# Kernel optimization log

Hardware: AMD Instinct MI355X
Metric: run time of the kernel (lower is better)

## Reference

```python
import jax, jax.numpy as jnp
import numpy as np

EPS_LN = 1e-5


def layer_norm(x, g, b):
    mu = jnp.mean(x, axis=-1, keepdims=True)
    var = jnp.mean((x - mu) ** 2, axis=-1, keepdims=True)
    return (x - mu) * jax.lax.rsqrt(var + EPS_LN) * g + b


def setup_inputs() -> dict:
    key = jax.random.key(0)
    ks = jax.random.split(key, 16)
    N, E, H, EA = 25000, 400000, 128, 1
    h = jax.random.normal(ks[0], (N, H), dtype=jnp.float32)
    coord = jax.random.normal(ks[1], (N, 3), dtype=jnp.float32)
    edge_index = jax.random.randint(ks[2], (2, E), 0, N, dtype=jnp.int64)
    edge_attr = jax.random.normal(ks[3], (E, EA), dtype=jnp.float32)

    def lin(k, fan_in, fan_out):
        lim = 1.0 / np.sqrt(fan_in)
        return jax.random.uniform(k, (fan_in, fan_out), jnp.float32, -lim, lim)

    in_edge = 2 * H + 1 + EA  # 258
    params = {
        'e_W1': lin(ks[4], in_edge, H), 'e_b1': jnp.zeros((H,), jnp.float32),
        'e_g1': jnp.ones((H,), jnp.float32), 'e_be1': jnp.zeros((H,), jnp.float32),
        'e_W2': lin(ks[5], H, H), 'e_b2': jnp.zeros((H,), jnp.float32),
        'e_g2': jnp.ones((H,), jnp.float32), 'e_be2': jnp.zeros((H,), jnp.float32),
        'n_W1': lin(ks[6], 2 * H, H), 'n_b1': jnp.zeros((H,), jnp.float32),
        'n_g1': jnp.ones((H,), jnp.float32), 'n_be1': jnp.zeros((H,), jnp.float32),
        'n_W2': lin(ks[7], H, H), 'n_b2': jnp.zeros((H,), jnp.float32),
        'c_W1': lin(ks[8], H, H), 'c_b1': jnp.zeros((H,), jnp.float32),
        'c_g1': jnp.ones((H,), jnp.float32), 'c_be1': jnp.zeros((H,), jnp.float32),
        # xavier_uniform with gain=0.001, no bias
        'c_W2': jax.random.uniform(ks[9], (H, 1), jnp.float32, -1.0, 1.0) * (0.001 * np.sqrt(6.0 / (H + 1))),
    }
    return dict(h=h, edge_index=edge_index, coord=coord, edge_attr=edge_attr, **params)


def reference(h, edge_index, coord, edge_attr,
              e_W1, e_b1, e_g1, e_be1, e_W2, e_b2, e_g2, e_be2,
              n_W1, n_b1, n_g1, n_be1, n_W2, n_b2,
              c_W1, c_b1, c_g1, c_be1, c_W2):
    N = h.shape[0]
    row, col = edge_index[0], edge_index[1]

    coord_diff = coord[row] - coord[col]                     # [E,3]
    radial = jnp.sum(coord_diff ** 2, axis=1, keepdims=True)  # [E,1]
    norm = jnp.sqrt(radial + 1e-8)
    coord_diff = coord_diff / (norm + 1.0)

    inp = jnp.concatenate([h[row], h[col], radial, edge_attr], axis=1)  # [E,258]
    x = jax.nn.silu(layer_norm(inp @ e_W1 + e_b1, e_g1, e_be1))
    edge_feat = jax.nn.silu(layer_norm(x @ e_W2 + e_b2, e_g2, e_be2))   # [E,H]

    cm = jax.nn.silu(layer_norm(edge_feat @ c_W1 + c_b1, c_g1, c_be1)) @ c_W2  # [E,1]
    trans = coord_diff * cm                                   # [E,3]

    coord_out = coord + jax.ops.segment_sum(trans, row, num_segments=N)
    agg = jax.ops.segment_sum(edge_feat, row, num_segments=N)  # [N,H]

    node_in = jnp.concatenate([h, agg], axis=1)               # [N,2H]
    out = jax.nn.silu(layer_norm(node_in @ n_W1 + n_b1, n_g1, n_be1)) @ n_W2 + n_b2
    out = h + out  # recurrent
    return out, coord_out
```

## Files before the change

kernel.cpp:

```cpp
#include <hip/hip_runtime.h>
#include <math.h>

#define H 128
#define KE 256
#define KN 256
#define XSTR 136
#define SSTR 132

typedef __attribute__((ext_vector_type(8))) short bf16x8;
typedef __attribute__((ext_vector_type(4))) float f32x4;

__device__ __forceinline__ float fast_rcp(float x) {
#if defined(__has_builtin) && __has_builtin(__builtin_amdgcn_rcpf)
    return __builtin_amdgcn_rcpf(x);
#else
    return 1.0f / x;
#endif
}
__device__ __forceinline__ float fast_rsq(float x) {
#if defined(__has_builtin) && __has_builtin(__builtin_amdgcn_rsqf)
    return __builtin_amdgcn_rsqf(x);
#else
    return rsqrtf(x);
#endif
}
__device__ __forceinline__ float fast_sqrt(float x) {
#if defined(__has_builtin) && __has_builtin(__builtin_amdgcn_sqrtf)
    return __builtin_amdgcn_sqrtf(x);
#else
    return sqrtf(x);
#endif
}

__device__ __forceinline__ float silu_f(float x) {
    return x * fast_rcp(1.0f + __expf(-x));
}

__device__ __forceinline__ unsigned short f2bf(float f) {
    unsigned int u = __float_as_uint(f);
    unsigned int r = u + 0x7FFFu + ((u >> 16) & 1u);
    return (unsigned short)(r >> 16);
}

__device__ __forceinline__ unsigned int pkbf(float a, float b) {
#if defined(__has_builtin)
#if __has_builtin(__builtin_amdgcn_cvt_pk_bf16_f32)
    typedef __attribute__((ext_vector_type(2))) __bf16 bf16x2_t;
    bf16x2_t v = __builtin_amdgcn_cvt_pk_bf16_f32(a, b);
    return *(unsigned int*)&v;
#else
    return (unsigned int)f2bf(a) | ((unsigned int)f2bf(b) << 16);
#endif
#else
    return (unsigned int)f2bf(a) | ((unsigned int)f2bf(b) << 16);
#endif
}

__device__ __forceinline__ float bflo(unsigned int w) { return __uint_as_float(w << 16); }
__device__ __forceinline__ float bfhi(unsigned int w) { return __uint_as_float(w & 0xFFFF0000u); }

__device__ __forceinline__ void atomic_pk_add_bf16(unsigned short* addr, unsigned int pkv) {
    asm volatile("global_atomic_pk_add_bf16 %0, %1, off"
                 :: "v"(addr), "v"(pkv) : "memory");
}

template<int CTRL>
__device__ __forceinline__ float dpp_add(float x) {
    int t = __builtin_amdgcn_update_dpp(0, __float_as_int(x), CTRL, 0xF, 0xF, true);
    return x + __int_as_float(t);
}
__device__ __forceinline__ float red16(float x) {
    x = dpp_add<0x128>(x);
    x = dpp_add<0x124>(x);
    x = dpp_add<0x122>(x);
    x = dpp_add<0x121>(x);
    return x;
}

__device__ __forceinline__ void wfrag(const float* __restrict__ W,
                                      unsigned short* __restrict__ Wf, int f) {
    int kb = f >> 9, rem = f & 511;
    int nt = rem >> 6, lane = rem & 63;
    int quad = lane >> 4, l15 = lane & 15;
    int n = nt * 16 + l15, k0 = kb * 32 + quad * 8;
    union { bf16x8 v; unsigned short u[8]; } pk;
    #pragma unroll
    for (int j = 0; j < 8; ++j) pk.u[j] = f2bf(W[(size_t)(k0 + j) * H + n]);
    *(bf16x8*)&Wf[(size_t)f * 8] = pk.v;
}

__global__ __launch_bounds__(256) void prep_all(
    const float* __restrict__ h, unsigned short* __restrict__ hb, int n4_h,
    float* __restrict__ aggz, int n4_agg,
    const float* __restrict__ coord, float* __restrict__ coord_out, int n_coord,
    const float* __restrict__ eW1, const float* __restrict__ eW2,
    const float* __restrict__ cW1, const float* __restrict__ nW1,
    const float* __restrict__ nW2,
    unsigned short* __restrict__ eW1f, unsigned short* __restrict__ eW2f,
    unsigned short* __restrict__ cW1f, unsigned short* __restrict__ nW1f,
    unsigned short* __restrict__ nW2f,
    int b0, int b1, int b2)
{
    int b = blockIdx.x;
    int t = threadIdx.x;
    if (b < b0) {
        int i = b * 256 + t;
        if (i < n4_h) {
            float4 f = ((const float4*)h)[i];
            ((uint2*)hb)[i] = make_uint2(pkbf(f.x, f.y), pkbf(f.z, f.w));
        }
    } else if (b < b1) {
        int i = (b - b0) * 256 + t;
        if (i < n4_agg) ((float4*)aggz)[i] = (float4){0.f, 0.f, 0.f, 0.f};
    } else if (b < b2) {
        int i = (b - b1) * 256 + t;
        if (i < n_coord) coord_out[i] = coord[i];
    } else {
        int idx = (b - b2) * 256 + t;
        if      (idx <  4096) wfrag(eW1, eW1f, idx);
        else if (idx <  8192) wfrag(nW1, nW1f, idx - 4096);
        else if (idx < 10240) wfrag(eW2, eW2f, idx - 8192);
        else if (idx < 12288) wfrag(cW1, cW1f, idx - 10240);
        else if (idx < 14336) wfrag(nW2, nW2f, idx - 12288);
    }
}

__global__ __launch_bounds__(256, 4) void proj_kernel(
    const unsigned short* __restrict__ hb,
    const unsigned short* __restrict__ eW1f,
    unsigned short* __restrict__ Pb, int N)
{
    __shared__ unsigned short Ys[4][16 * 256];

    const int wv = threadIdx.x >> 6;
    const int lane = threadIdx.x & 63;
    const int l15 = lane & 15, quad = lane >> 4;
    const int gn0 = (blockIdx.x * 4 + wv) * 16;
    unsigned short* Y = &Ys[wv][0];

    if (gn0 >= N) return;
    int nl = gn0 + l15; if (nl >= N) nl = N - 1;

    f32x4 a1[8], a2[8];
    #pragma unroll
    for (int nt = 0; nt < 8; ++nt) {
        a1[nt] = (f32x4){0.f, 0.f, 0.f, 0.f};
        a2[nt] = (f32x4){0.f, 0.f, 0.f, 0.f};
    }

    for (int kb = 0; kb < 4; ++kb) {
        int ko = kb * 32 + quad * 8;
        bf16x8 af = *(const bf16x8*)(hb + (size_t)nl * H + ko);
        const unsigned short* bp1 = eW1f + ((size_t)kb * 8) * 512 + (size_t)lane * 8;
        const unsigned short* bp2 = eW1f + ((size_t)(kb + 4) * 8) * 512 + (size_t)lane * 8;
        #pragma unroll
        for (int nt = 0; nt < 8; ++nt) {
            bf16x8 b1 = *(const bf16x8*)(bp1 + (size_t)nt * 512);
            bf16x8 b2 = *(const bf16x8*)(bp2 + (size_t)nt * 512);
            a1[nt] = __builtin_amdgcn_mfma_f32_16x16x32_bf16(af, b1, a1[nt], 0, 0, 0);
            a2[nt] = __builtin_amdgcn_mfma_f32_16x16x32_bf16(af, b2, a2[nt], 0, 0, 0);
        }
    }

    #pragma unroll
    for (int nt = 0; nt < 8; ++nt) {
        int c = nt * 16 + l15;
        #pragma unroll
        for (int r = 0; r < 4; ++r) {
            int rr = quad * 4 + r;
            Y[rr * 256 + c]       = f2bf(a1[nt][r]);
            Y[rr * 256 + 128 + c] = f2bf(a2[nt][r]);
        }
    }

    const int m = lane >> 2, part = lane & 3;
    int gm = gn0 + m; if (gm >= N) gm = N - 1;
    #pragma unroll
    for (int j = 0; j < 8; ++j) {
        uint4 v = *(const uint4*)&Y[m * 256 + part * 64 + j * 8];
        *(uint4*)(Pb + (size_t)gm * 256 + part * 64 + j * 8) = v;
    }
}

__device__ __forceinline__ void ln_silu_store1(
    f32x4* acc, const float* __restrict__ bias, const float* __restrict__ g,
    const float* __restrict__ be, unsigned short* X, int l15, int quad)
{
    float s[4] = {0,0,0,0}, q[4] = {0,0,0,0};
    #pragma unroll
    for (int nt = 0; nt < 8; ++nt) {
        float b = bias[nt * 16 + l15];
        #pragma unroll
        for (int r = 0; r < 4; ++r) {
            float x = acc[nt][r] + b; acc[nt][r] = x; s[r] += x; q[r] += x * x;
        }
    }
    #pragma unroll
    for (int r = 0; r < 4; ++r) { s[r] = red16(s[r]); q[r] = red16(q[r]); }
    #pragma unroll
    for (int r = 0; r < 4; ++r) {
        float mu = s[r] * 0.0078125f, v = q[r] * 0.0078125f - mu * mu;
        s[r] = mu; q[r] = fast_rsq(v + 1e-5f);
    }
    #pragma unroll
    for (int nt = 0; nt < 8; ++nt) {
        float gg = g[nt * 16 + l15], bb = be[nt * 16 + l15];
        #pragma unroll
        for (int r = 0; r < 4; ++r) {
            float a = q[r] * gg, c = bb - s[r] * a;
            float y = silu_f(fmaf(acc[nt][r], a, c));
            acc[nt][r] = y;
            X[(quad * 4 + r) * XSTR + nt * 16 + l15] = f2bf(y);
        }
    }
}

__global__ __launch_bounds__(64, 4) void edge_kernel(
    const unsigned short* __restrict__ Pb, const int* __restrict__ ei,
    const float* __restrict__ coord, const float* __restrict__ eattr,
    const float* __restrict__ eW1,
    const float* __restrict__ eb1, const float* __restrict__ eg1, const float* __restrict__ ebe1,
    const unsigned short* __restrict__ eW2f,
    const float* __restrict__ eb2, const float* __restrict__ eg2, const float* __restrict__ ebe2,
    const unsigned short* __restrict__ cW1f,
    const float* __restrict__ cb1, const float* __restrict__ cg1, const float* __restrict__ cbe1,
    const float* __restrict__ cW2,
    unsigned short* __restrict__ aggb, float* __restrict__ coord_out, int E)
{
    __shared__ float S[16 * SSTR];
    unsigned short* X = (unsigned short*)S;

    const int lane = threadIdx.x;
    const int l15 = lane & 15, quad = lane >> 4;
    const int ge0 = blockIdx.x * 16;

    int el  = ge0 + l15;
    int elc = (el < E) ? el : (E - 1);
    int rowl = ei[elc], coll = ei[E + elc];
    float dx = coord[rowl * 3 + 0] - coord[coll * 3 + 0];
    float dy = coord[rowl * 3 + 1] - coord[coll * 3 + 1];
    float dz = coord[rowl * 3 + 2] - coord[coll * 3 + 2];
    float radial = dx * dx + dy * dy + dz * dz;
    float inv = fast_rcp(fast_sqrt(radial + 1e-8f) + 1.0f);
    float cdx = dx * inv, cdy = dy * inv, cdz = dz * inv;
    float ea = eattr[elc];

    {
        const int m = lane >> 2, part = lane & 3;
        int row_m = __shfl(rowl, m, 64);
        int col_m = __shfl(coll, m, 64);
        const unsigned short* p1 = Pb + (size_t)row_m * 256 + part * 32;
        const unsigned short* p2 = Pb + (size_t)col_m * 256 + 128 + part * 32;
        #pragma unroll
        for (int j = 0; j < 4; ++j) {
            uint4 a = *(const uint4*)(p1 + j * 8);
            uint4 b = *(const uint4*)(p2 + j * 8);
            float4 v0, v1;
            v0.x = bflo(a.x) + bflo(b.x); v0.y = bfhi(a.x) + bfhi(b.x);
            v0.z = bflo(a.y) + bflo(b.y); v0.w = bfhi(a.y) + bfhi(b.y);
            v1.x = bflo(a.z) + bflo(b.z); v1.y = bfhi(a.z) + bfhi(b.z);
            v1.z = bflo(a.w) + bflo(b.w); v1.w = bfhi(a.w) + bfhi(b.w);
            *(float4*)&S[m * SSTR + part * 32 + j * 8]     = v0;
            *(float4*)&S[m * SSTR + part * 32 + j * 8 + 4] = v1;
        }
    }

    f32x4 acc[8];
    {
        float rad_r[4], ea_r[4];
        #pragma unroll
        for (int r = 0; r < 4; ++r) {
            rad_r[r] = __shfl(radial, quad * 4 + r, 64);
            ea_r[r]  = __shfl(ea,     quad * 4 + r, 64);
        }
        #pragma unroll
        for (int nt = 0; nt < 8; ++nt) {
            float w256 = eW1[256 * H + nt * 16 + l15];
            float w257 = eW1[257 * H + nt * 16 + l15];
            #pragma unroll
            for (int r = 0; r < 4; ++r) {
                float base = S[(quad * 4 + r) * SSTR + nt * 16 + l15];
                acc[nt][r] = base + rad_r[r] * w256 + ea_r[r] * w257;
            }
        }
    }

    ln_silu_store1(acc, eb1, eg1, ebe1, X, l15, quad);

    f32x4 ac2[8];
    #pragma unroll
    for (int nt = 0; nt < 8; ++nt) ac2[nt] = (f32x4){0.f, 0.f, 0.f, 0.f};
    for (int kb = 0; kb < 4; ++kb) {
        bf16x8 af = *(const bf16x8*)&X[l15 * XSTR + kb * 32 + quad * 8];
        const unsigned short* bp = eW2f + ((size_t)kb * 8) * 512 + (size_t)lane * 8;
        #pragma unroll
        for (int nt = 0; nt < 8; ++nt) {
            bf16x8 bf = *(const bf16x8*)(bp + (size_t)nt * 512);
            ac2[nt] = __builtin_amdgcn_mfma_f32_16x16x32_bf16(af, bf, ac2[nt], 0, 0, 0);
        }
    }

    ln_silu_store1(ac2, eb2, eg2, ebe2, X, l15, quad);

    {
        int rowm[4];
        #pragma unroll
        for (int r = 0; r < 4; ++r) rowm[r] = __shfl(rowl, quad * 4 + r, 64);
        #pragma unroll
        for (int c4 = 0; c4 < 4; ++c4) {
            #pragma unroll
            for (int r = 0; r < 4; ++r) {
                int geh = ge0 + quad * 4 + r;
                if (geh < E) {
                    unsigned int pkv =
                        *(const unsigned int*)&X[(quad * 4 + r) * XSTR + c4 * 32 + 2 * l15];
                    atomic_pk_add_bf16(aggb + (size_t)rowm[r] * H + c4 * 32 + 2 * l15, pkv);
                }
            }
        }
    }

    f32x4 acc3[8];
    #pragma unroll
    for (int nt = 0; nt < 8; ++nt) acc3[nt] = (f32x4){0.f, 0.f, 0.f, 0.f};
    for (int kb = 0; kb < 4; ++kb) {
        bf16x8 af = *(const bf16x8*)&X[l15 * XSTR + kb * 32 + quad * 8];
        const unsigned short* bp = cW1f + ((size_t)kb * 8) * 512 + (size_t)lane * 8;
        #pragma unroll
        for (int nt = 0; nt < 8; ++nt) {
            bf16x8 bf = *(const bf16x8*)(bp + (size_t)nt * 512);
            acc3[nt] = __builtin_amdgcn_mfma_f32_16x16x32_bf16(af, bf, acc3[nt], 0, 0, 0);
        }
    }

    {
        float s[4] = {0,0,0,0}, q[4] = {0,0,0,0};
        #pragma unroll
        for (int nt = 0; nt < 8; ++nt) {
            float b = cb1[nt * 16 + l15];
            #pragma unroll
            for (int r = 0; r < 4; ++r) {
                float x = acc3[nt][r] + b; acc3[nt][r] = x; s[r] += x; q[r] += x * x;
            }
        }
        #pragma unroll
        for (int r = 0; r < 4; ++r) { s[r] = red16(s[r]); q[r] = red16(q[r]); }
        #pragma unroll
        for (int r = 0; r < 4; ++r) {
            float mu = s[r] * 0.0078125f, v = q[r] * 0.0078125f - mu * mu;
            s[r] = mu; q[r] = fast_rsq(v + 1e-5f);
        }
        float cm[4] = {0,0,0,0};
        #pragma unroll
        for (int nt = 0; nt < 8; ++nt) {
            float gg = cg1[nt * 16 + l15], bb = cbe1[nt * 16 + l15];
            float w2 = cW2[nt * 16 + l15];
            #pragma unroll
            for (int r = 0; r < 4; ++r) {
                float a = q[r] * gg, c = bb - s[r] * a;
                cm[r] += silu_f(fmaf(acc3[nt][r], a, c)) * w2;
            }
        }
        #pragma unroll
        for (int r = 0; r < 4; ++r) cm[r] = red16(cm[r]);
        #pragma unroll
        for (int r = 0; r < 4; ++r) {
            int src = quad * 4 + r;
            float cdxr = __shfl(cdx, src, 64);
            float cdyr = __shfl(cdy, src, 64);
            float cdzr = __shfl(cdz, src, 64);
            int rw = __shfl(rowl, src, 64);
            float comp = (l15 == 0) ? cdxr : ((l15 == 1) ? cdyr : cdzr);
            int geh = ge0 + src;
            if (l15 < 3 && geh < E)
                atomicAdd(&coord_out[(size_t)rw * 3 + l15], comp * cm[r]);
        }
    }
}

__global__ __launch_bounds__(256, 4) void node_kernel(
    const unsigned short* __restrict__ hb, const float* __restrict__ h,
    const unsigned short* __restrict__ aggb,
    const unsigned short* __restrict__ nW1f,
    const float* __restrict__ nb1, const float* __restrict__ ng1, const float* __restrict__ nbe1,
    const unsigned short* __restrict__ nW2f, const float* __restrict__ nb2,
    float* __restrict__ out, int N)
{
    __shared__ unsigned short Xs[4][16 * XSTR];

    const int wv   = threadIdx.x >> 6;
    const int lane = threadIdx.x & 63;
    const int l15 = lane & 15, quad = lane >> 4;
    const int gn0 = (blockIdx.x * 4 + wv) * 16;
    unsigned short* X = &Xs[wv][0];

    if (gn0 >= N) return;
    int nl = gn0 + l15; if (nl >= N) nl = N - 1;

    f32x4 acc[8];
    #pragma unroll
    for (int nt = 0; nt < 8; ++nt) acc[nt] = (f32x4){0.f, 0.f, 0.f, 0.f};

    for (int kb = 0; kb < 8; ++kb) {
        int ko = (kb & 3) * 32 + quad * 8;
        const unsigned short* src = (kb < 4) ? hb : aggb;
        bf16x8 af = *(const bf16x8*)(src + (size_t)nl * H + ko);
        const unsigned short* bp = nW1f + ((size_t)kb * 8) * 512 + (size_t)lane * 8;
        #pragma unroll
        for (int nt = 0; nt < 8; ++nt) {
            bf16x8 bf = *(const bf16x8*)(bp + (size_t)nt * 512);
            acc[nt] = __builtin_amdgcn_mfma_f32_16x16x32_bf16(af, bf, acc[nt], 0, 0, 0);
        }
    }

    ln_silu_store1(acc, nb1, ng1, nbe1, X, l15, quad);

    f32x4 ac2[8];
    #pragma unroll
    for (int nt = 0; nt < 8; ++nt) ac2[nt] = (f32x4){0.f, 0.f, 0.f, 0.f};
    for (int kb = 0; kb < 4; ++kb) {
        bf16x8 af = *(const bf16x8*)&X[l15 * XSTR + kb * 32 + quad * 8];
        const unsigned short* bp = nW2f + ((size_t)kb * 8) * 512 + (size_t)lane * 8;
        #pragma unroll
        for (int nt = 0; nt < 8; ++nt) {
            bf16x8 bf = *(const bf16x8*)(bp + (size_t)nt * 512);
            ac2[nt] = __builtin_amdgcn_mfma_f32_16x16x32_bf16(af, bf, ac2[nt], 0, 0, 0);
        }
    }

    #pragma unroll
    for (int nt = 0; nt < 8; ++nt) {
        float b = nb2[nt * 16 + l15];
        #pragma unroll
        for (int r = 0; r < 4; ++r) {
            int gn = gn0 + quad * 4 + r;
            if (gn < N) {
                size_t idx = (size_t)gn * H + nt * 16 + l15;
                out[idx] = ac2[nt][r] + b + h[idx];
            }
        }
    }
}

extern "C" void kernel_launch(void* const* d_in, const int* in_sizes, int n_in,
                              void* d_out, int out_size, void* d_ws, size_t ws_size,
                              hipStream_t stream) {
    const float* h     = (const float*)d_in[0];
    const int*   ei    = (const int*)d_in[1];
    const float* coord = (const float*)d_in[2];
    const float* eattr = (const float*)d_in[3];
    const float* eW1   = (const float*)d_in[4];
    const float* eb1   = (const float*)d_in[5];
    const float* eg1   = (const float*)d_in[6];
    const float* ebe1  = (const float*)d_in[7];
    const float* eW2   = (const float*)d_in[8];
    const float* eb2   = (const float*)d_in[9];
    const float* eg2   = (const float*)d_in[10];
    const float* ebe2  = (const float*)d_in[11];
    const float* nW1   = (const float*)d_in[12];
    const float* nb1   = (const float*)d_in[13];
    const float* ng1   = (const float*)d_in[14];
    const float* nbe1  = (const float*)d_in[15];
    const float* nW2   = (const float*)d_in[16];
    const float* nb2   = (const float*)d_in[17];
    const float* cW1   = (const float*)d_in[18];
    const float* cb1   = (const float*)d_in[19];
    const float* cg1   = (const float*)d_in[20];
    const float* cbe1  = (const float*)d_in[21];
    const float* cW2   = (const float*)d_in[22];

    const int N = in_sizes[0] / H;
    const int E = in_sizes[1] / 2;

    float* out       = (float*)d_out;
    float* coord_out = out + (size_t)N * H;

    char* ws = (char*)d_ws;
    size_t o = 0;
    unsigned short* aggb = (unsigned short*)(ws + o); o += (size_t)N * H * 2;
    unsigned short* hb   = (unsigned short*)(ws + o); o += (size_t)N * H * 2;
    unsigned short* Pb   = (unsigned short*)(ws + o); o += (size_t)N * 256 * 2;
    unsigned short* eW1f = (unsigned short*)(ws + o); o += (size_t)H * KE * 2;
    unsigned short* eW2f = (unsigned short*)(ws + o); o += (size_t)H * H * 2;
    unsigned short* cW1f = (unsigned short*)(ws + o); o += (size_t)H * H * 2;
    unsigned short* nW1f = (unsigned short*)(ws + o); o += (size_t)H * KN * 2;
    unsigned short* nW2f = (unsigned short*)(ws + o); o += (size_t)H * H * 2;

    const int n4_h   = N * H / 4;
    const int n4_agg = N * H / 8;
    const int n_co   = N * 3;
    const int b0 = (n4_h   + 255) / 256;
    const int b1 = b0 + (n4_agg + 255) / 256;
    const int b2 = b1 + (n_co   + 255) / 256;
    const int bw = (4096 + 4096 + 2048 + 2048 + 2048 + 255) / 256;
    prep_all<<<b2 + bw, 256, 0, stream>>>(
        h, hb, n4_h, (float*)aggb, n4_agg, coord, coord_out, n_co,
        eW1, eW2, cW1, nW1, nW2,
        eW1f, eW2f, cW1f, nW1f, nW2f, b0, b1, b2);

    proj_kernel<<<(N + 63) / 64, 256, 0, stream>>>(hb, eW1f, Pb, N);

    edge_kernel<<<(E + 15) / 16, 64, 0, stream>>>(
        Pb, ei, coord, eattr,
        eW1, eb1, eg1, ebe1,
        eW2f, eb2, eg2, ebe2,
        cW1f, cb1, cg1, cbe1, cW2,
        aggb, coord_out, E);

    node_kernel<<<(N + 63) / 64, 256, 0, stream>>>(
        hb, h, aggb, nW1f, nb1, ng1, nbe1, nW2f, nb2, out, N);
}
```

Before: 301.2 us.

## Pack two waves per edge block and stage layer-1 input as bf16

The edge kernel now runs two independent 16-edge waves per 128-thread block, each with its own bf16 LDS tile, instead of one wave per block. The radial and edge_attr terms of the first layer are folded in during the gather, and the pre-activation is stored as bf16 in the shared X buffer rather than as an fp32 staging array. This shrinks LDS per wave and raises launch bounds to allow more resident waves. In exchange the layer-1 pre-activation is rounded to bf16 before layer norm, which costs some accuracy.

```diff
diff --git a/kernel.cpp b/kernel.cpp
--- a/kernel.cpp
+++ b/kernel.cpp
@@ -5,7 +5,6 @@
 #define KE 256
 #define KN 256
 #define XSTR 136
-#define SSTR 132
 
 typedef __attribute__((ext_vector_type(8))) short bf16x8;
 typedef __attribute__((ext_vector_type(4))) float f32x4;
@@ -58,6 +57,9 @@
 
 __device__ __forceinline__ float bflo(unsigned int w) { return __uint_as_float(w << 16); }
 __device__ __forceinline__ float bfhi(unsigned int w) { return __uint_as_float(w & 0xFFFF0000u); }
+__device__ __forceinline__ float bfu(unsigned short u) {
+    return __uint_as_float((unsigned int)u << 16);
+}
 
 __device__ __forceinline__ void atomic_pk_add_bf16(unsigned short* addr, unsigned int pkv) {
     asm volatile("global_atomic_pk_add_bf16 %0, %1, off"
@@ -215,7 +217,7 @@
     }
 }
 
-__global__ __launch_bounds__(64, 4) void edge_kernel(
+__global__ __launch_bounds__(128, 8) void edge_kernel(
     const unsigned short* __restrict__ Pb, const int* __restrict__ ei,
     const float* __restrict__ coord, const float* __restrict__ eattr,
     const float* __restrict__ eW1,
@@ -227,12 +229,15 @@
     const float* __restrict__ cW2,
     unsigned short* __restrict__ aggb, float* __restrict__ coord_out, int E)
 {
-    __shared__ float S[16 * SSTR];
-    unsigned short* X = (unsigned short*)S;
-
-    const int lane = threadIdx.x;
+    __shared__ unsigned short Xs[2][16 * XSTR];
+
+    const int wv   = threadIdx.x >> 6;
+    const int lane = threadIdx.x & 63;
     const int l15 = lane & 15, quad = lane >> 4;
-    const int ge0 = blockIdx.x * 16;
+    const int ge0 = (blockIdx.x * 2 + wv) * 16;
+    unsigned short* X = &Xs[wv][0];
+
+    if (ge0 >= E) return;
 
     int el  = ge0 + l15;
     int elc = (el < E) ? el : (E - 1);
@@ -247,44 +252,45 @@
 
     {
         const int m = lane >> 2, part = lane & 3;
-        int row_m = __shfl(rowl, m, 64);
-        int col_m = __shfl(coll, m, 64);
+        int row_m   = __shfl(rowl,   m, 64);
+        int col_m   = __shfl(coll,   m, 64);
+        float rad_m = __shfl(radial, m, 64);
+        float ea_m  = __shfl(ea,     m, 64);
         const unsigned short* p1 = Pb + (size_t)row_m * 256 + part * 32;
         const unsigned short* p2 = Pb + (size_t)col_m * 256 + 128 + part * 32;
+        const float* w6 = eW1 + 256 * H + part * 32;
+        const float* w7 = eW1 + 257 * H + part * 32;
+        unsigned short* Xrow = X + m * XSTR + part * 32;
         #pragma unroll
         for (int j = 0; j < 4; ++j) {
             uint4 a = *(const uint4*)(p1 + j * 8);
             uint4 b = *(const uint4*)(p2 + j * 8);
-            float4 v0, v1;
-            v0.x = bflo(a.x) + bflo(b.x); v0.y = bfhi(a.x) + bfhi(b.x);
-            v0.z = bflo(a.y) + bflo(b.y); v0.w = bfhi(a.y) + bfhi(b.y);
-            v1.x = bflo(a.z) + bflo(b.z); v1.y = bfhi(a.z) + bfhi(b.z);
-            v1.z = bflo(a.w) + bflo(b.w); v1.w = bfhi(a.w) + bfhi(b.w);
-            *(float4*)&S[m * SSTR + part * 32 + j * 8]     = v0;
-            *(float4*)&S[m * SSTR + part * 32 + j * 8 + 4] = v1;
+            float4 wA = *(const float4*)(w6 + j * 8);
+            float4 wB = *(const float4*)(w6 + j * 8 + 4);
+            float4 uA = *(const float4*)(w7 + j * 8);
+            float4 uB = *(const float4*)(w7 + j * 8 + 4);
+            float v0 = bflo(a.x) + bflo(b.x) + rad_m * wA.x + ea_m * uA.x;
+            float v1 = bfhi(a.x) + bfhi(b.x) + rad_m * wA.y + ea_m * uA.y;
+            float v2 = bflo(a.y) + bflo(b.y) + rad_m * wA.z + ea_m * uA.z;
+            float v3 = bfhi(a.y) + bfhi(b.y) + rad_m * wA.w + ea_m * uA.w;
+            float v4 = bflo(a.z) + bflo(b.z) + rad_m * wB.x + ea_m * uB.x;
+            float v5 = bfhi(a.z) + bfhi(b.z) + rad_m * wB.y + ea_m * uB.y;
+            float v6 = bflo(a.w) + bflo(b.w) + rad_m * wB.z + ea_m * uB.z;
+            float v7 = bfhi(a.w) + bfhi(b.w) + rad_m * wB.w + ea_m * uB.w;
+            uint4 o;
+            o.x = pkbf(v0, v1); o.y = pkbf(v2, v3);
+            o.z = pkbf(v4, v5); o.w = pkbf(v6, v7);
+            *(uint4*)(Xrow + j * 8) = o;
         }
     }
 
     f32x4 acc[8];
-    {
-        float rad_r[4], ea_r[4];
-        #pragma unroll
-        for (int r = 0; r < 4; ++r) {
-            rad_r[r] = __shfl(radial, quad * 4 + r, 64);
-            ea_r[r]  = __shfl(ea,     quad * 4 + r, 64);
-        }
-        #pragma unroll
-        for (int nt = 0; nt < 8; ++nt) {
-            float w256 = eW1[256 * H + nt * 16 + l15];
-            float w257 = eW1[257 * H + nt * 16 + l15];
-            #pragma unroll
-            for (int r = 0; r < 4; ++r) {
-                float base = S[(quad * 4 + r) * SSTR + nt * 16 + l15];
-                acc[nt][r] = base + rad_r[r] * w256 + ea_r[r] * w257;
-            }
-        }
-    }
-
+    #pragma unroll
+    for (int nt = 0; nt < 8; ++nt) {
+        #pragma unroll
+        for (int r = 0; r < 4; ++r)
+            acc[nt][r] = bfu(X[(quad * 4 + r) * XSTR + nt * 16 + l15]);
+    }
     ln_silu_store1(acc, eb1, eg1, ebe1, X, l15, quad);
 
     f32x4 ac2[8];
@@ -500,7 +506,7 @@
 
     proj_kernel<<<(N + 63) / 64, 256, 0, stream>>>(hb, eW1f, Pb, N);
 
-    edge_kernel<<<(E + 15) / 16, 64, 0, stream>>>(
+    edge_kernel<<<(E + 31) / 32, 128, 0, stream>>>(
         Pb, ei, coord, eattr,
         eW1, eb1, eg1, ebe1,
         eW2f, eb2, eg2, ebe2,
```

Result: slower. 370.0 us (+22.8%).
